# Kernel tuning notes

Hardware: AMD Instinct MI355X
Metric: run time of the kernel (lower is better)

## Reference

```python
import jax, jax.numpy as jnp
import numpy as np

TAL = 0.07
LOSS_WEIGHT = 1.0


def setup_inputs() -> dict:
    key = jax.random.key(0)
    k1, k2 = jax.random.split(key)
    feature = jax.random.normal(k1, (8192, 1024), dtype=jnp.float32)
    # labels all >= 1 so the foreground mask (label > 0) selects every row,
    # matching the original's fea = feature[label > 0] with a static shape.
    label = jax.random.randint(k2, (8192,), 1, 80, dtype=jnp.int32)
    return {"feature": feature, "label": label}


def reference(feature, label):
    # foreground=True and all labels > 0 -> fea = feature, lab = label
    fea = feature
    lab = label
    n = fea.shape[0]

    norm = jnp.linalg.norm(fea, axis=1)                      # [n]
    # ex[i, j] = <fea_i, fea_j> / (tal * ||fea_i|| * ||fea_j||)
    ex = (fea @ fea.T) / (TAL * norm[:, None] * norm[None, :])  # [n, n]

    # d_all = exp(ex); column sum pos_val + neg_val == sum_i d_all[i, j].
    # -log(d_all[i, j] / colsum_j) = logsumexp_i(ex[:, j]) - ex[i, j]
    log_colsum = jax.nn.logsumexp(ex, axis=0)                # [n]

    pos = lab[:, None] == lab[None, :]                       # pos[i, j]: lab_i == lab_j
    n_pos = jnp.sum(pos, axis=0).astype(ex.dtype)            # per-anchor positive count

    per_pair = jnp.where(pos, log_colsum[None, :] - ex, jnp.zeros((), ex.dtype))
    loss_anc = jnp.sum(per_pair, axis=0) / n_pos             # [n], mean over positives
    loss = jnp.sum(loss_anc)
    return LOSS_WEIGHT * loss / n
```

## Files before the change

kernel.cpp:

```cpp
#include <hip/hip_runtime.h>

#define TAL 0.07f
constexpr int N = 8192;
constexpr int D = 1024;
constexpr int NB = 64;
constexpr int NTILES = NB * (NB + 1) / 2;
constexpr int TPX = NTILES / 8;

typedef __bf16 bf16x8 __attribute__((ext_vector_type(8)));
typedef float f32x4 __attribute__((ext_vector_type(4)));

#define AS1 __attribute__((address_space(1)))
#define AS3 __attribute__((address_space(3)))

#define WAIT_VM(n) asm volatile("s_waitcnt vmcnt(" #n ")" ::: "memory")
#define WAIT_LGKM0 asm volatile("s_waitcnt lgkmcnt(0)" ::: "memory")
#define SCHED_FENCE __builtin_amdgcn_sched_barrier(0)
#define SBAR __builtin_amdgcn_s_barrier()

static __device__ __forceinline__ ushort f2bf(float x) {
    union { float f; uint32_t u; } c; c.f = x;
    uint32_t u = c.u;
    uint32_t r = (u + 0x7FFFu + ((u >> 16) & 1u)) >> 16;
    return (ushort)r;
}

__global__ __launch_bounds__(256) void prep_kernel(const float* __restrict__ F,
                                                   const int* __restrict__ lab,
                                                   ushort* __restrict__ Fb,
                                                   float* __restrict__ ascale,
                                                   int* __restrict__ hist) {
    int row = blockIdx.x * 4 + (threadIdx.x >> 6);
    int lane = threadIdx.x & 63;
    const float4* src = (const float4*)(F + (size_t)row * D);
    ushort4* dst = (ushort4*)(Fb + (size_t)row * D);
    float local = 0.f;
    #pragma unroll
    for (int it = 0; it < 4; ++it) {
        float4 v = src[it * 64 + lane];
        ushort4 o;
        o.x = f2bf(v.x); o.y = f2bf(v.y); o.z = f2bf(v.z); o.w = f2bf(v.w);
        dst[it * 64 + lane] = o;
        local += v.x*v.x + v.y*v.y + v.z*v.z + v.w*v.w;
    }
    #pragma unroll
    for (int off = 32; off; off >>= 1) local += __shfl_xor(local, off);
    if (lane == 0) {
        ascale[row] = rsqrtf(TAL * local);
        atomicAdd(&hist[lab[row]], 1);
    }
}

#define BM 128
#define BN 128
#define BK 32
#define TILE (BM * BK)
#define NSTEP (D / BK)

__global__ __launch_bounds__(256, 3) void gemm_kernel(const ushort* __restrict__ Fb,
                                                      const float* __restrict__ ascale,
                                                      const int* __restrict__ lab,
                                                      float* __restrict__ gSumE,
                                                      float* __restrict__ gSumP) {
    __shared__ ushort sA[3][TILE];
    __shared__ ushort sB[3][TILE];
    __shared__ float rScale[BM], cScale[BN];
    __shared__ int rLab[BM], cLab[BN];

    int kblk = blockIdx.x;
    int b = (kblk & 7) * TPX + (kblk >> 3);

    int bi = (int)((sqrtf(8.f * (float)b + 1.f) - 1.f) * 0.5f);
    while ((bi + 1) * (bi + 2) / 2 <= b) ++bi;
    while (bi * (bi + 1) / 2 > b) --bi;
    int bj = b - bi * (bi + 1) / 2;
    bool offdiag = (bi != bj);

    int I0 = bi * BM, J0 = bj * BN;
    int t = threadIdx.x;
    int lane = t & 63, w = t >> 6;
    int wr = w >> 1, wc = w & 1;

    if (t < 128) { rScale[t] = ascale[I0 + t]; rLab[t] = lab[I0 + t]; }
    else { int u = t - 128; cScale[u] = ascale[J0 + u]; cLab[u] = lab[J0 + u]; }

    f32x4 acc[4][4];
    #pragma unroll
    for (int m = 0; m < 4; ++m)
        #pragma unroll
        for (int n = 0; n < 4; ++n)
            acc[m][n] = {0.f, 0.f, 0.f, 0.f};

    int r0 = (w * 2 + 0) * 16 + (lane >> 2);
    int r1 = (w * 2 + 1) * 16 + (lane >> 2);
    int ce = (((lane & 3) ^ ((lane >> 3) & 3))) * 8;
    const ushort* srcA0 = Fb + (size_t)(I0 + r0) * D + ce;
    const ushort* srcA1 = Fb + (size_t)(I0 + r1) * D + ce;
    const ushort* srcB0 = Fb + (size_t)(J0 + r0) * D + ce;
    const ushort* srcB1 = Fb + (size_t)(J0 + r1) * D + ce;
    ushort* sAf = &sA[0][0];
    ushort* sBf = &sB[0][0];
    int d0 = (w * 2 + 0) * 512;
    int d1 = (w * 2 + 1) * 512;

#define STAGE(c, koff) do {                                                                              \
    __builtin_amdgcn_global_load_lds((const AS1 void*)(srcA0 + (koff)), (AS3 void*)(sAf + (c)*TILE + d0), 16, 0, 0); \
    __builtin_amdgcn_global_load_lds((const AS1 void*)(srcA1 + (koff)), (AS3 void*)(sAf + (c)*TILE + d1), 16, 0, 0); \
    __builtin_amdgcn_global_load_lds((const AS1 void*)(srcB0 + (koff)), (AS3 void*)(sBf + (c)*TILE + d0), 16, 0, 0); \
    __builtin_amdgcn_global_load_lds((const AS1 void*)(srcB1 + (koff)), (AS3 void*)(sBf + (c)*TILE + d1), 16, 0, 0); \
} while (0)

    int fr = lane & 15;
    int cs = ((lane >> 4) ^ ((lane >> 1) & 3)) * 8;

#define DSREAD(AF, BF, cb) do {                                                        \
    const ushort* a_ = sAf + (cb) * TILE;                                              \
    const ushort* b_ = sBf + (cb) * TILE;                                              \
    _Pragma("unroll")                                                                  \
    for (int m = 0; m < 4; ++m)                                                        \
        AF[m] = *(const bf16x8*)(a_ + (wr * 64 + m * 16 + fr) * BK + cs);              \
    _Pragma("unroll")                                                                  \
    for (int n = 0; n < 4; ++n)                                                        \
        BF[n] = *(const bf16x8*)(b_ + (wc * 64 + n * 16 + fr) * BK + cs);              \
} while (0)

#define MFMA16(AF, BF) do {                                                            \
    _Pragma("unroll")                                                                  \
    for (int m = 0; m < 4; ++m)                                                        \
        _Pragma("unroll")                                                              \
        for (int n = 0; n < 4; ++n)                                                    \
            acc[m][n] = __builtin_amdgcn_mfma_f32_16x16x32_bf16(AF[m], BF[n], acc[m][n], 0, 0, 0); \
} while (0)

#define PITER(rb, sb, CA, CB, NA, NB_, tt) do {                                        \
    STAGE(sb, ((tt) + 2) * BK);                                                        \
    WAIT_VM(4); SCHED_FENCE; SBAR; SCHED_FENCE;                                        \
    DSREAD(NA, NB_, rb);                                                               \
    MFMA16(CA, CB);                                                                    \
    WAIT_LGKM0; SCHED_FENCE;                                                           \
} while (0)

    STAGE(0, 0 * BK);
    STAGE(1, 1 * BK);
    __syncthreads();
    bf16x8 afA[4], bfA[4], afB[4], bfB[4];
    DSREAD(afA, bfA, 0);
    WAIT_LGKM0; SCHED_FENCE;

    for (int s = 0; s < NSTEP - 2; s += 6) {
        PITER(1, 2, afA, bfA, afB, bfB, s);
        PITER(2, 0, afB, bfB, afA, bfA, s + 1);
        PITER(0, 1, afA, bfA, afB, bfB, s + 2);
        PITER(1, 2, afB, bfB, afA, bfA, s + 3);
        PITER(2, 0, afA, bfA, afB, bfB, s + 4);
        PITER(0, 1, afB, bfB, afA, bfA, s + 5);
    }
    WAIT_VM(0); SCHED_FENCE; SBAR; SCHED_FENCE;
    DSREAD(afB, bfB, 1);
    MFMA16(afA, bfA);
    MFMA16(afB, bfB);

    float rs[16]; int rl[16];
    int rbase = wr * 64 + (lane >> 4) * 4;
    #pragma unroll
    for (int m = 0; m < 4; ++m)
        #pragma unroll
        for (int r = 0; r < 4; ++r) {
            rs[m * 4 + r] = rScale[rbase + m * 16 + r];
            rl[m * 4 + r] = rLab[rbase + m * 16 + r];
        }

    const float CSH = 1.0f / TAL;
    float colE[4], colP[4], rowE[16], rowP[16];
    #pragma unroll
    for (int n = 0; n < 4; ++n) { colE[n] = 0.f; colP[n] = 0.f; }
    #pragma unroll
    for (int q = 0; q < 16; ++q) { rowE[q] = 0.f; rowP[q] = 0.f; }

    #pragma unroll
    for (int n = 0; n < 4; ++n) {
        int jl = wc * 64 + n * 16 + fr;
        float aj = cScale[jl];
        int lj = cLab[jl];
        #pragma unroll
        for (int m = 0; m < 4; ++m)
            #pragma unroll
            for (int r = 0; r < 4; ++r) {
                float ex = acc[m][n][r] * rs[m * 4 + r] * aj;
                float e = __expf(ex - CSH);
                float p = (rl[m * 4 + r] == lj) ? ex : 0.f;
                colE[n] += e; colP[n] += p;
                rowE[m * 4 + r] += e; rowP[m * 4 + r] += p;
            }
    }

    #pragma unroll
    for (int n = 0; n < 4; ++n) {
        float se = colE[n], sp = colP[n];
        se += __shfl_xor(se, 16); se += __shfl_xor(se, 32);
        sp += __shfl_xor(sp, 16); sp += __shfl_xor(sp, 32);
        if (lane < 16) {
            int jl = wc * 64 + n * 16 + lane;
            atomicAdd(&gSumE[J0 + jl], se);
            atomicAdd(&gSumP[J0 + jl], sp);
        }
    }

    if (offdiag) {
        #pragma unroll
        for (int q = 0; q < 16; ++q) {
            float se = rowE[q], sp = rowP[q];
            se += __shfl_xor(se, 1); se += __shfl_xor(se, 2);
            se += __shfl_xor(se, 4); se += __shfl_xor(se, 8);
            sp += __shfl_xor(sp, 1); sp += __shfl_xor(sp, 2);
            sp += __shfl_xor(sp, 4); sp += __shfl_xor(sp, 8);
            if ((lane & 15) == 0) {
                int row = rbase + (q >> 2) * 16 + (q & 3);
                atomicAdd(&gSumE[I0 + row], se);
                atomicAdd(&gSumP[I0 + row], sp);
            }
        }
    }
}

__global__ __launch_bounds__(256) void finalize_kernel(const float* __restrict__ gSumE,
                                                       const float* __restrict__ gSumP,
                                                       const int* __restrict__ lab,
                                                       const int* __restrict__ hist,
                                                       float* __restrict__ out) {
    int t = threadIdx.x;
    int j = blockIdx.x * 256 + t;
    const float CSH = 1.0f / TAL;
    float np = (float)hist[lab[j]];
    float local = CSH + logf(gSumE[j]) - gSumP[j] / np;
    #pragma unroll
    for (int off = 32; off; off >>= 1) local += __shfl_xor(local, off);
    __shared__ float red[4];
    if ((t & 63) == 0) red[t >> 6] = local;
    __syncthreads();
    if (t == 0) atomicAdd(out, (red[0] + red[1] + red[2] + red[3]) / (float)N);
}

extern "C" void kernel_launch(void* const* d_in, const int* in_sizes, int n_in,
                              void* d_out, int out_size, void* d_ws, size_t ws_size,
                              hipStream_t stream) {
    const float* F = (const float*)d_in[0];
    const int* lab = (const int*)d_in[1];
    float* out = (float*)d_out;
    char* ws = (char*)d_ws;

    const size_t FB_BYTES = (size_t)N * D * 2;
    ushort* Fb    = (ushort*)ws;
    float* ascale = (float*)(ws + FB_BYTES);
    float* gSumE  = (float*)(ws + FB_BYTES + 32768);
    float* gSumP  = (float*)(ws + FB_BYTES + 65536);
    int*   hist   = (int*)  (ws + FB_BYTES + 98304);

    hipMemsetAsync(ws + FB_BYTES + 32768, 0, 65536 + 512, stream);
    hipMemsetAsync(d_out, 0, sizeof(float), stream);

    prep_kernel<<<N / 4, 256, 0, stream>>>(F, lab, Fb, ascale, hist);
    gemm_kernel<<<NTILES, 256, 0, stream>>>(Fb, ascale, lab, gSumE, gSumP);
    finalize_kernel<<<N / 256, 256, 0, stream>>>(gSumE, gSumP, lab, hist, out);
}
```

Measured before the change: 231.3 us.

## Drop memsets, move histogram into single-block finalize, add MFMA priority hints

Removes the two hipMemsetAsync calls by zeroing the accumulation buffers inside prep_kernel, and moves the label histogram from global atomics into a single 1024-thread finalize block that writes the result directly. In the GEMM main loop it removes the explicit lgkmcnt(0) wait and scheduling fence after each step and wraps the MFMA batch in s_setprio raise/lower. This cuts launch and memset overhead and global atomics; the single-block finalize serializes the tail reduction, and dropping the wait leaves LDS-read ordering to the compiler.

```diff
diff --git a/kernel.cpp b/kernel.cpp
--- a/kernel.cpp
+++ b/kernel.cpp
@@ -14,7 +14,6 @@
 #define AS3 __attribute__((address_space(3)))
 
 #define WAIT_VM(n) asm volatile("s_waitcnt vmcnt(" #n ")" ::: "memory")
-#define WAIT_LGKM0 asm volatile("s_waitcnt lgkmcnt(0)" ::: "memory")
 #define SCHED_FENCE __builtin_amdgcn_sched_barrier(0)
 #define SBAR __builtin_amdgcn_s_barrier()
 
@@ -26,10 +25,12 @@
 }
 
 __global__ __launch_bounds__(256) void prep_kernel(const float* __restrict__ F,
-                                                   const int* __restrict__ lab,
                                                    ushort* __restrict__ Fb,
                                                    float* __restrict__ ascale,
-                                                   int* __restrict__ hist) {
+                                                   float* __restrict__ gSumZ) {
+    int gid = blockIdx.x * 256 + threadIdx.x;
+    if (gid < 16384) gSumZ[gid] = 0.f;
+
     int row = blockIdx.x * 4 + (threadIdx.x >> 6);
     int lane = threadIdx.x & 63;
     const float4* src = (const float4*)(F + (size_t)row * D);
@@ -45,10 +46,7 @@
     }
     #pragma unroll
     for (int off = 32; off; off >>= 1) local += __shfl_xor(local, off);
-    if (lane == 0) {
-        ascale[row] = rsqrtf(TAL * local);
-        atomicAdd(&hist[lab[row]], 1);
-    }
+    if (lane == 0) ascale[row] = rsqrtf(TAL * local);
 }
 
 #define BM 128
@@ -136,8 +134,9 @@
     STAGE(sb, ((tt) + 2) * BK);                                                        \
     WAIT_VM(4); SCHED_FENCE; SBAR; SCHED_FENCE;                                        \
     DSREAD(NA, NB_, rb);                                                               \
+    __builtin_amdgcn_s_setprio(1);                                                     \
     MFMA16(CA, CB);                                                                    \
-    WAIT_LGKM0; SCHED_FENCE;                                                           \
+    __builtin_amdgcn_s_setprio(0);                                                     \
 } while (0)
 
     STAGE(0, 0 * BK);
@@ -145,7 +144,6 @@
     __syncthreads();
     bf16x8 afA[4], bfA[4], afB[4], bfB[4];
     DSREAD(afA, bfA, 0);
-    WAIT_LGKM0; SCHED_FENCE;
 
     for (int s = 0; s < NSTEP - 2; s += 6) {
         PITER(1, 2, afA, bfA, afB, bfB, s);
@@ -223,22 +221,38 @@
     }
 }
 
-__global__ __launch_bounds__(256) void finalize_kernel(const float* __restrict__ gSumE,
-                                                       const float* __restrict__ gSumP,
-                                                       const int* __restrict__ lab,
-                                                       const int* __restrict__ hist,
-                                                       float* __restrict__ out) {
+__global__ __launch_bounds__(1024) void finalize_kernel(const float* __restrict__ gSumE,
+                                                        const float* __restrict__ gSumP,
+                                                        const int* __restrict__ lab,
+                                                        float* __restrict__ out) {
+    __shared__ int h[80];
+    __shared__ float red[16];
     int t = threadIdx.x;
-    int j = blockIdx.x * 256 + t;
+    if (t < 80) h[t] = 0;
+    __syncthreads();
+    #pragma unroll
+    for (int it = 0; it < N / 1024; ++it)
+        atomicAdd(&h[lab[it * 1024 + t]], 1);
+    __syncthreads();
+
     const float CSH = 1.0f / TAL;
-    float np = (float)hist[lab[j]];
-    float local = CSH + logf(gSumE[j]) - gSumP[j] / np;
+    float local = 0.f;
+    #pragma unroll
+    for (int it = 0; it < N / 1024; ++it) {
+        int j = it * 1024 + t;
+        float np = (float)h[lab[j]];
+        local += CSH + logf(gSumE[j]) - gSumP[j] / np;
+    }
     #pragma unroll
     for (int off = 32; off; off >>= 1) local += __shfl_xor(local, off);
-    __shared__ float red[4];
     if ((t & 63) == 0) red[t >> 6] = local;
     __syncthreads();
-    if (t == 0) atomicAdd(out, (red[0] + red[1] + red[2] + red[3]) / (float)N);
+    if (t == 0) {
+        float s = 0.f;
+        #pragma unroll
+        for (int i = 0; i < 16; ++i) s += red[i];
+        out[0] = s / (float)N;
+    }
 }
 
 extern "C" void kernel_launch(void* const* d_in, const int* in_sizes, int n_in,
@@ -254,12 +268,8 @@
     float* ascale = (float*)(ws + FB_BYTES);
     float* gSumE  = (float*)(ws + FB_BYTES + 32768);
     float* gSumP  = (float*)(ws + FB_BYTES + 65536);
-    int*   hist   = (int*)  (ws + FB_BYTES + 98304);
-
-    hipMemsetAsync(ws + FB_BYTES + 32768, 0, 65536 + 512, stream);
-    hipMemsetAsync(d_out, 0, sizeof(float), stream);
-
-    prep_kernel<<<N / 4, 256, 0, stream>>>(F, lab, Fb, ascale, hist);
+
+    prep_kernel<<<N / 4, 256, 0, stream>>>(F, Fb, ascale, gSumE);
     gemm_kernel<<<NTILES, 256, 0, stream>>>(Fb, ascale, lab, gSumE, gSumP);
-    finalize_kernel<<<N / 256, 256, 0, stream>>>(gSumE, gSumP, lab, hist, out);
-}
+    finalize_kernel<<<1, 1024, 0, stream>>>(gSumE, gSumP, lab, out);
+}
```

New measurement: 212.5 us. 8.1% less time.
